# Optimization experiments

Hardware: AMD Instinct MI355X
Metric: run time of the kernel (lower is better)

Reference implementation:

```python
import jax, jax.numpy as jnp
import numpy as np

B, N, D = 4, 1024, 1024
H = 16
RS, RC = 32, 32
MLP = int(D * 4.0)
EPS = 1e-6


def _ln(x):
    # LayerNorm with no scale/bias (flax defaults: eps=1e-6)
    m = jnp.mean(x, axis=-1, keepdims=True)
    v = jnp.mean(jnp.square(x - m), axis=-1, keepdims=True)
    return (x - m) * jax.lax.rsqrt(v + EPS)


def _rms(x, scale):
    rms = jnp.sqrt(jnp.mean(jnp.square(x), axis=-1, keepdims=True) + EPS)
    return scale * x / rms


def _modulate(x, shift, scale):
    return x * (1 + scale[:, None]) + shift[:, None]


def setup_inputs() -> dict:
    key = jax.random.key(0)
    ks = jax.random.split(key, 20)
    s = 0.02
    return {
        'x': jax.random.normal(ks[0], (B, N, D), jnp.float32),
        'c': jax.random.normal(ks[1], (B, D), jnp.float32),
        'cls_token': jax.random.normal(ks[2], (B, D), jnp.float32),
        'Wc': jax.random.normal(ks[3], (D, 6 * D), jnp.float32) * s,
        'bc': jax.random.normal(ks[4], (6 * D,), jnp.float32) * s,
        'Wqkv': jax.random.normal(ks[5], (D, 3 * D), jnp.float32) * s,
        'bqkv': jnp.zeros((3 * D,), jnp.float32),
        'Wo': jax.random.normal(ks[6], (D, D), jnp.float32) * s,
        'bo': jnp.zeros((D,), jnp.float32),
        'A_s': jax.random.normal(ks[7], (D, RS), jnp.float32) * s,
        'B_s': jax.random.normal(ks[8], (RS, D), jnp.float32) * s,
        'rms_s_scale': jnp.ones((D,), jnp.float32),
        'C_r': jax.random.normal(ks[9], (D, RC), jnp.float32) * s,
        'D_r': jax.random.normal(ks[10], (RC, D), jnp.float32) * s,
        'rms_c_scale': jnp.ones((D,), jnp.float32),
        'W1': jax.random.normal(ks[11], (D, MLP), jnp.float32) * s,
        'b1': jnp.zeros((MLP,), jnp.float32),
        'W2': jax.random.normal(ks[12], (MLP, D), jnp.float32) * s,
        'b2': jnp.zeros((D,), jnp.float32),
    }


def reference(x, c, cls_token, Wc, bc, Wqkv, bqkv, Wo, bo, A_s, B_s,
              rms_s_scale, C_r, D_r, rms_c_scale, W1, b1, W2, b2):
    hd = D // H
    # AdaLN conditioning
    c_proj = jax.nn.silu(c) @ Wc + bc                    # (B, 6D)
    shift_a, scale_a, gate_a, shift_m, scale_m, gate_m = jnp.split(c_proj, 6, axis=-1)

    # Self-attention branch
    x_norm = _modulate(_ln(x), shift_a, scale_a)         # (B, N, D)
    qkv = x_norm @ Wqkv + bqkv                           # (B, N, 3D)
    q, k, v = jnp.split(qkv, 3, axis=-1)
    q = q.reshape(B, N, H, hd).transpose(0, 2, 1, 3)     # (B, H, N, hd)
    k = k.reshape(B, N, H, hd).transpose(0, 2, 1, 3)
    v = v.reshape(B, N, H, hd).transpose(0, 2, 1, 3)
    attn_w = jax.nn.softmax(jnp.einsum('bhqd,bhkd->bhqk', q, k) * hd ** (-0.5), axis=-1)
    attn_out = jnp.einsum('bhqk,bhkd->bhqd', attn_w, v)
    attn_out = attn_out.transpose(0, 2, 1, 3).reshape(B, N, D)
    attn_out = attn_out @ Wo + bo
    Y = x + gate_a[:, None] * attn_out

    # Self-gram low-rank branch (residual)
    gram_s = (x @ A_s) @ B_s                             # (B, N, D)
    X_prime = _rms(gram_s, rms_s_scale) + Y

    # Cross-gram branch via CLS token (no residual)
    u_c = cls_token[:, :, None] * C_r[None]              # (B, D, RC)
    v_c = jnp.einsum('bnd,bdr->bnr', X_prime, u_c)       # (B, N, RC)
    gram_c = v_c @ D_r                                   # (B, N, D)
    Z = _rms(gram_c, rms_c_scale)

    # MLP branch
    z_norm = _modulate(_ln(Z), shift_m, scale_m)
    h = jax.nn.gelu(z_norm @ W1 + b1) @ W2 + b2
    return Z + gate_m[:, None] * h
```

## Files before the change

### kernel.cpp

```cpp
#include <hip/hip_runtime.h>
#include <stdint.h>

typedef float  f32x4  __attribute__((ext_vector_type(4)));
typedef int    i32x4  __attribute__((ext_vector_type(4)));
typedef __bf16 bf16x4 __attribute__((ext_vector_type(4)));

#define D_    1024
#define SIXD  6144
#define QSCALE 0.18033688011112042f

#define BAR() asm volatile("s_barrier" ::: "memory")

__device__ __forceinline__ void mfma16(const i32x4 &a, const i32x4 &b, f32x4 &c) {
  asm("v_mfma_f32_16x16x32_bf16 %0, %1, %2, %0" : "+v"(c) : "v"(a), "v"(b));
}

__device__ __forceinline__ void gload_lds16(const void* g, void* l) {
  __builtin_amdgcn_global_load_lds(
      (const __attribute__((address_space(1))) uint32_t*)g,
      (__attribute__((address_space(3))) uint32_t*)l, 16, 0, 0);
}

__global__ __launch_bounds__(256)
void cond_gemm(const float* __restrict__ c, const float* __restrict__ Wc,
               const float* __restrict__ bc, float* __restrict__ cproj)
{
  __shared__ float sc[4096];
  __shared__ float tp[8][4][32];
  int tid = threadIdx.x;
  for (int i = tid; i < 4096; i += 256) {
    float v = c[i];
    sc[i] = v / (1.f + __expf(-v));
  }
  __syncthreads();
  int colo = tid & 31, kseg = tid >> 5;
  int col = blockIdx.x * 32 + colo;
  float a0 = 0.f, a1 = 0.f, a2 = 0.f, a3 = 0.f;
  for (int k = kseg * 128; k < kseg * 128 + 128; k++) {
    float w = Wc[(size_t)k * SIXD + col];
    a0 += sc[k] * w; a1 += sc[1024 + k] * w;
    a2 += sc[2048 + k] * w; a3 += sc[3072 + k] * w;
  }
  tp[kseg][0][colo] = a0; tp[kseg][1][colo] = a1;
  tp[kseg][2][colo] = a2; tp[kseg][3][colo] = a3;
  __syncthreads();
  if (kseg == 0) {
#pragma unroll
    for (int b = 0; b < 4; b++) {
      float s = bc[col];
#pragma unroll
      for (int g = 0; g < 8; g++) s += tp[g][b][colo];
      cproj[b * SIXD + col] = s;
    }
  }
}

__global__ __launch_bounds__(256)
void transpose_all(const float* __restrict__ Wqkv, const float* __restrict__ Wo,
                   const float* __restrict__ W1, const float* __restrict__ W2,
                   __bf16* __restrict__ Wqkvt, __bf16* __restrict__ Wot,
                   __bf16* __restrict__ W1t, __bf16* __restrict__ W2t)
{
  __shared__ __bf16 t[64][65];
  int bid = blockIdx.x;
  const float* W; __bf16* Wt; int Kdim, Ndim, lb;
  if (bid < 768)       { W = Wqkv; Wt = Wqkvt; Kdim = 1024; Ndim = 3072; lb = bid; }
  else if (bid < 1024) { W = Wo;   Wt = Wot;   Kdim = 1024; Ndim = 1024; lb = bid - 768; }
  else if (bid < 2048) { W = W1;   Wt = W1t;   Kdim = 1024; Ndim = 4096; lb = bid - 1024; }
  else                 { W = W2;   Wt = W2t;   Kdim = 4096; Ndim = 1024; lb = bid - 2048; }
  int ntn = Ndim >> 6;
  int kt = lb / ntn, nt = lb % ntn;
  int tid = threadIdx.x;
  const float* src = W + (size_t)(kt * 64) * Ndim + nt * 64;
#pragma unroll
  for (int i = 0; i < 4; i++) {
    int k = i * 16 + (tid >> 4);
    int c4 = tid & 15;
    float4 v = ((const float4*)(src + (size_t)k * Ndim))[c4];
    t[k][c4 * 4 + 0] = (__bf16)v.x; t[k][c4 * 4 + 1] = (__bf16)v.y;
    t[k][c4 * 4 + 2] = (__bf16)v.z; t[k][c4 * 4 + 3] = (__bf16)v.w;
  }
  __syncthreads();
  __bf16* dst = Wt + (size_t)(nt * 64) * Kdim + kt * 64;
  int n = tid >> 2, ks = (tid & 3) * 16;
  bf16x4 o0, o1, o2, o3;
#pragma unroll
  for (int j = 0; j < 4; j++) {
    o0[j] = t[ks + j][n];      o1[j] = t[ks + 4 + j][n];
    o2[j] = t[ks + 8 + j][n];  o3[j] = t[ks + 12 + j][n];
  }
  __bf16* dp = dst + (size_t)n * Kdim + ks;
  *(bf16x4*)(dp) = o0; *(bf16x4*)(dp + 4) = o1;
  *(bf16x4*)(dp + 8) = o2; *(bf16x4*)(dp + 12) = o3;
}

__global__ __launch_bounds__(256)
void transpose_v(const __bf16* __restrict__ qkv, __bf16* __restrict__ Vt)
{
  __shared__ __bf16 t[32][33];
  int bid = blockIdx.x;
  int dt = bid & 1, nt = (bid >> 1) & 31, bh = bid >> 6;
  int b = bh >> 4, h = bh & 15;
  int x = threadIdx.x & 31, yq = threadIdx.x >> 5;
  const __bf16* src = qkv + ((size_t)(b * 1024 + nt * 32)) * 3072 + 2048 + h * 64 + dt * 32;
#pragma unroll
  for (int i = 0; i < 4; i++) {
    int row = yq * 4 + i;
    t[row][x] = src[(size_t)row * 3072 + x];
  }
  __syncthreads();
  __bf16* dst = Vt + ((size_t)(bh * 64 + dt * 32)) * 1024 + nt * 32;
#pragma unroll
  for (int i = 0; i < 4; i++) {
    int drow = yq * 4 + i;
    dst[(size_t)drow * 1024 + x] = t[x][drow];
  }
}

__global__ __launch_bounds__(256)
void ln_mod(const float* __restrict__ X, const float* __restrict__ cproj,
            int shift_off, int scale_off, __bf16* __restrict__ Out)
{
  int row = blockIdx.x;
  int b = row >> 10;
  int tid = threadIdx.x;
  const float4* xr = (const float4*)(X + (size_t)row * D_);
  float4 v = xr[tid];
  float s  = v.x + v.y + v.z + v.w;
  float s2 = v.x * v.x + v.y * v.y + v.z * v.z + v.w * v.w;
#pragma unroll
  for (int off = 1; off < 64; off <<= 1) {
    s  += __shfl_xor(s,  off, 64);
    s2 += __shfl_xor(s2, off, 64);
  }
  __shared__ float red[8];
  int wave = tid >> 6, lane = tid & 63;
  if (lane == 0) { red[wave] = s; red[4 + wave] = s2; }
  __syncthreads();
  s  = red[0] + red[1] + red[2] + red[3];
  s2 = red[4] + red[5] + red[6] + red[7];
  float mean = s * (1.f / D_);
  float var  = s2 * (1.f / D_) - mean * mean;
  float rstd = rsqrtf(var + 1e-6f);
  const float4* sh = (const float4*)(cproj + b * SIXD + shift_off);
  const float4* sc = (const float4*)(cproj + b * SIXD + scale_off);
  float4 shv = sh[tid], scv = sc[tid];
  bf16x4 o;
  o[0] = (__bf16)((v.x - mean) * rstd * (1.f + scv.x) + shv.x);
  o[1] = (__bf16)((v.y - mean) * rstd * (1.f + scv.y) + shv.y);
  o[2] = (__bf16)((v.z - mean) * rstd * (1.f + scv.z) + shv.z);
  o[3] = (__bf16)((v.w - mean) * rstd * (1.f + scv.w) + shv.w);
  *(bf16x4*)(Out + (size_t)row * D_ + tid * 4) = o;
}

template<int EPI, int NBUF>
__global__ __launch_bounds__(256)
void gemm_bt(const __bf16* __restrict__ A, const __bf16* __restrict__ Bt,
             const float* __restrict__ bias, const float* __restrict__ cproj,
             int gate_off, const float* __restrict__ resid,
             void* __restrict__ Cout, void* __restrict__ Cout2,
             void* __restrict__ Cout3, void* __restrict__ Cout4,
             int M, int N, int K, int SK)
{
  __shared__ __align__(16) __bf16 As[NBUF * 128 * 32];
  __shared__ __align__(16) __bf16 Bs[NBUF * 128 * 32];
  const int PD = NBUF - 1;
  int tilesN = N >> 7, tilesM = M >> 7;
  int npersk = tilesM * tilesN;
  int sk = blockIdx.x / npersk;
  int rest = blockIdx.x % npersk;
  int cpx = npersk >> 3;
  rest = (rest & 7) * cpx + (rest >> 3);
  int bm = rest / tilesN, bn = rest % tilesN;
  int Klen = K / SK, Kstart = sk * Klen;

  int tid = threadIdx.x;
  int lane = tid & 63, wave = tid >> 6;
  int lr = lane & 15, lg = lane >> 4;
  int wm = (wave >> 1) << 6, wn = (wave & 1) << 6;

  f32x4 acc[4][4] = {};

  int sr = tid >> 2, skb = tid & 3;
  int scol = ((skb ^ ((sr >> 1) & 3)) * 8);
  const __bf16* pa = A + (size_t)((bm << 7) + sr) * K + Kstart + scol;
  const __bf16* pb = Bt + (size_t)((bn << 7) + sr) * K + Kstart + scol;
  const size_t rstep = (size_t)64 * K;
  __bf16* la = As + tid * 8;
  __bf16* lb = Bs + tid * 8;

  auto STAGE = [&](int buf, int k0) {
    int bo = buf * 4096;
    gload_lds16(pa + k0, la + bo);
    gload_lds16(pa + rstep + k0, la + bo + 2048);
    gload_lds16(pb + k0, lb + bo);
    gload_lds16(pb + rstep + k0, lb + bo + 2048);
  };

  int nt = Klen >> 5;
#pragma unroll
  for (int p = 0; p < PD; p++) STAGE(p, p * 32);

  for (int t = 0; t < nt; t++) {
    if (t + PD < nt) STAGE((t + PD) % NBUF, (t + PD) * 32);
    int ahead = nt - 1 - t; if (ahead > PD) ahead = PD;
    if (ahead >= 3)      asm volatile("s_waitcnt vmcnt(12)" ::: "memory");
    else if (ahead == 2) asm volatile("s_waitcnt vmcnt(8)" ::: "memory");
    else if (ahead == 1) asm volatile("s_waitcnt vmcnt(4)" ::: "memory");
    else                 asm volatile("s_waitcnt vmcnt(0)" ::: "memory");
    BAR();
    const __bf16* Ac = As + (t % NBUF) * 4096;
    const __bf16* Bc = Bs + (t % NBUF) * 4096;
    i32x4 af[4], bfv[4];
#pragma unroll
    for (int m = 0; m < 4; m++) {
      int row = wm + m * 16 + lr;
      af[m] = *(const i32x4*)(Ac + row * 32 + ((lg ^ ((row >> 1) & 3)) * 8));
    }
#pragma unroll
    for (int n = 0; n < 4; n++) {
      int row = wn + n * 16 + lr;
      bfv[n] = *(const i32x4*)(Bc + row * 32 + ((lg ^ ((row >> 1) & 3)) * 8));
    }
    asm volatile("s_waitcnt lgkmcnt(0)" ::: "memory");
    __builtin_amdgcn_sched_barrier(0);
    BAR();
    __builtin_amdgcn_s_setprio(1);
#pragma unroll
    for (int m = 0; m < 4; m++)
#pragma unroll
      for (int n = 0; n < 4; n++)
        mfma16(af[m], bfv[n], acc[m][n]);
    __builtin_amdgcn_s_setprio(0);
  }
  asm volatile("s_waitcnt vmcnt(0)" ::: "memory");
  asm volatile("s_nop 7\n\ts_nop 7" ::);

  __bf16* Pp = nullptr;
  if (EPI == 3) {
    if (sk == 0)      Pp = (__bf16*)Cout;
    else if (sk == 1) Pp = (__bf16*)Cout2;
    else if (sk == 2) Pp = (__bf16*)Cout3;
    else              Pp = (__bf16*)Cout4;
  }

  int row0 = (bm << 7) + wm;
  int col0 = (bn << 7) + wn;
#pragma unroll
  for (int m = 0; m < 4; m++) {
#pragma unroll
    for (int n = 0; n < 4; n++) {
      int cc = col0 + n * 16 + lr;
      float bv = (EPI == 3) ? 0.f : bias[cc];
#pragma unroll
      for (int r = 0; r < 4; r++) {
        int row = row0 + m * 16 + (lg << 2) + r;
        float v = acc[m][n][r] + bv;
        size_t idx = (size_t)row * N + cc;
        if (EPI == 0) {
          ((__bf16*)Cout)[idx] = (__bf16)v;
        } else if (EPI == 1) {
          int b = row >> 10;
          float g = cproj[b * SIXD + gate_off + cc];
          ((float*)Cout)[idx] = resid[idx] + g * v;
        } else if (EPI == 2) {
          float u = 0.7978845608028654f * (v + 0.044715f * v * v * v);
          u = fminf(fmaxf(u, -15.f), 15.f);
          float e = __expf(2.f * u);
          float th = (e - 1.f) / (e + 1.f);
          ((__bf16*)Cout)[idx] = (__bf16)(0.5f * v * (1.f + th));
        } else if (EPI == 4) {
          float scq = (cc < 1024) ? QSCALE : 1.f;
          ((__bf16*)Cout)[idx] = (__bf16)(v * scq);
        } else {
          Pp[idx] = (__bf16)v;
        }
      }
    }
  }
}

__global__ __launch_bounds__(256)
void reduce_w2(const __bf16* __restrict__ P0, const __bf16* __restrict__ P1,
               const __bf16* __restrict__ P2, const __bf16* __restrict__ P3,
               const float* __restrict__ bias, const float* __restrict__ cproj,
               float* __restrict__ Out)
{
  int row = blockIdx.x;
  int b = row >> 10;
  int tid = threadIdx.x;
  size_t base = (size_t)row * D_ + tid * 4;
  bf16x4 a0 = *(const bf16x4*)(P0 + base);
  bf16x4 a1 = *(const bf16x4*)(P1 + base);
  bf16x4 a2 = *(const bf16x4*)(P2 + base);
  bf16x4 a3 = *(const bf16x4*)(P3 + base);
  f32x4 s;
#pragma unroll
  for (int i = 0; i < 4; i++)
    s[i] = ((float)a0[i] + (float)a1[i]) + ((float)a2[i] + (float)a3[i]);
  f32x4 bz = *(const f32x4*)(bias + tid * 4);
  f32x4 g  = *(const f32x4*)(cproj + b * SIXD + 5120 + tid * 4);
  f32x4 z  = *(const f32x4*)(Out + base);
  *(f32x4*)(Out + base) = z + g * (s + bz);
}

__global__ __launch_bounds__(512, 4)
void attn_flash(const __bf16* __restrict__ qkv, const __bf16* __restrict__ Vt,
                __bf16* __restrict__ O)
{
  __shared__ __align__(16) __bf16 Kl[2][64 * 64];
  __shared__ __align__(16) __bf16 Vl[2][64 * 64];
  __shared__ __align__(16) __bf16 Pl[8][16 * 64];

  int bid = ((blockIdx.x & 7) << 6) | (blockIdx.x >> 3);
  int qt = bid & 7, h = (bid >> 3) & 15, b = bid >> 7;
  int tid = threadIdx.x, wave = tid >> 6, lane = tid & 63;
  int lr = lane & 15, lg = lane >> 4;

  size_t tok0 = (size_t)b * 1024;
  int qrow = qt * 128 + wave * 16 + lr;
  const __bf16* qptr = qkv + (tok0 + qrow) * 3072 + h * 64;
  i32x4 qf0 = *(const i32x4*)(qptr + lg * 8);
  i32x4 qf1 = *(const i32x4*)(qptr + 32 + lg * 8);

  float l_acc[4] = {0.f, 0.f, 0.f, 0.f};
  f32x4 oacc[4] = {};

  const __bf16* kbase = qkv + tok0 * 3072 + 1024 + h * 64;
  const __bf16* vbase = Vt + ((size_t)(b * 16 + h) * 64) * 1024;

  int skey = tid >> 3, sdb = tid & 7;
  const __bf16* ksrc = kbase + (size_t)skey * 3072 + ((sdb ^ (skey & 7)) * 8);
  const __bf16* vsrc = vbase + (size_t)skey * 1024 + ((sdb ^ (skey & 7)) * 8);
  __bf16* klp = &Kl[0][0] + tid * 8;
  __bf16* vlp = &Vl[0][0] + tid * 8;
  __bf16* pl = &Pl[wave][0];

  auto STAGE = [&](int buf, int kk) {
    gload_lds16(ksrc + (size_t)kk * 3072, klp + buf * 4096);
    gload_lds16(vsrc + kk, vlp + buf * 4096);
  };

  STAGE(0, 0);
  int cur = 0;
  for (int k0 = 0; k0 < 1024; k0 += 64) {
    int kn = (k0 + 64 < 1024) ? (k0 + 64) : k0;
    STAGE(cur ^ 1, kn);
    asm volatile("s_waitcnt vmcnt(2)" ::: "memory");
    BAR();
    const __bf16* K_ = &Kl[cur][0];
    const __bf16* V_ = &Vl[cur][0];

    f32x4 s[4];
    __builtin_amdgcn_s_setprio(1);
#pragma unroll
    for (int n = 0; n < 4; n++) {
      int key = n * 16 + lr;
      int kx = key & 7;
      i32x4 kf0 = *(const i32x4*)(K_ + key * 64 + ((lg ^ kx) * 8));
      i32x4 kf1 = *(const i32x4*)(K_ + key * 64 + (((4 + lg) ^ kx) * 8));
      f32x4 sa = {0.f, 0.f, 0.f, 0.f};
      mfma16(qf0, kf0, sa);
      mfma16(qf1, kf1, sa);
      s[n] = sa;
    }
    __builtin_amdgcn_s_setprio(0);

#pragma unroll
    for (int n = 0; n < 4; n++)
#pragma unroll
      for (int r = 0; r < 4; r++)
        s[n][r] = exp2f(s[n][r]);
#pragma unroll
    for (int r = 0; r < 4; r++)
      l_acc[r] += (s[0][r] + s[1][r]) + (s[2][r] + s[3][r]);

#pragma unroll
    for (int n = 0; n < 4; n++)
#pragma unroll
      for (int r = 0; r < 4; r++) {
        int prow = lg * 4 + r;
        int key = n * 16 + lr;
        int idx = prow * 64 + (((key >> 3) ^ (prow & 7)) * 8) + (key & 7);
        pl[idx] = (__bf16)s[n][r];
      }
    asm volatile("s_waitcnt lgkmcnt(0)" ::: "memory");
    __builtin_amdgcn_sched_barrier(0);
    i32x4 pf0 = *(const i32x4*)(pl + lr * 64 + ((lg ^ (lr & 7)) * 8));
    i32x4 pf1 = *(const i32x4*)(pl + lr * 64 + (((4 + lg) ^ (lr & 7)) * 8));

    __builtin_amdgcn_s_setprio(1);
#pragma unroll
    for (int dt = 0; dt < 4; dt++) {
      int vrow = dt * 16 + lr, rx = vrow & 7;
      i32x4 vf0 = *(const i32x4*)(V_ + vrow * 64 + ((lg ^ rx) * 8));
      i32x4 vf1 = *(const i32x4*)(V_ + vrow * 64 + (((4 + lg) ^ rx) * 8));
      mfma16(pf0, vf0, oacc[dt]);
      mfma16(pf1, vf1, oacc[dt]);
    }
    __builtin_amdgcn_s_setprio(0);
    asm volatile("s_waitcnt lgkmcnt(0)" ::: "memory");
    __builtin_amdgcn_sched_barrier(0);
    BAR();
    cur ^= 1;
  }
  asm volatile("s_waitcnt vmcnt(0)" ::: "memory");
  asm volatile("s_nop 7\n\ts_nop 7" ::);

  float rinv[4];
#pragma unroll
  for (int r = 0; r < 4; r++) {
    float v = l_acc[r];
#pragma unroll
    for (int off = 1; off < 16; off <<= 1) v += __shfl_xor(v, off, 64);
    rinv[r] = 1.f / v;
  }

  int orow = qt * 128 + wave * 16 + (lg << 2);
#pragma unroll
  for (int dt = 0; dt < 4; dt++)
#pragma unroll
    for (int r = 0; r < 4; r++) {
      float v = oacc[dt][r] * rinv[r];
      O[(tok0 + orow + r) * 1024 + h * 64 + dt * 16 + lr] = (__bf16)v;
    }
}

__global__ __launch_bounds__(256)
void gram_fused(const float* __restrict__ X, const float* __restrict__ Y,
                const float* __restrict__ cls,
                const float* __restrict__ A_s, const float* __restrict__ B_s,
                const float* __restrict__ rms_s,
                const float* __restrict__ C_r, const float* __restrict__ D_r,
                const float* __restrict__ rms_c,
                const float* __restrict__ cproj,
                float* __restrict__ Z, __bf16* __restrict__ Znorm)
{
  __shared__ float xs[4][D_];
  __shared__ float tp[8][4][32];
  __shared__ float t1[4][32];
  __shared__ float red[4][4];
  __shared__ float red2[4][4][2];
  int row0 = blockIdx.x * 4;
  int b = row0 >> 10;
  int tid = threadIdx.x;
  int wv = tid >> 6;

  f32x4 cv = *(const f32x4*)(cls + (size_t)b * D_ + tid * 4);
  f32x4 yv[4];
#pragma unroll
  for (int rr = 0; rr < 4; rr++) {
    ((f32x4*)xs[rr])[tid] = *(const f32x4*)(X + (size_t)(row0 + rr) * D_ + tid * 4);
    yv[rr] = *(const f32x4*)(Y + (size_t)(row0 + rr) * D_ + tid * 4);
  }
  __syncthreads();

  {
    int r = tid & 31, seg = tid >> 5;
    float a0 = 0.f, a1 = 0.f, a2 = 0.f, a3 = 0.f;
    const float* ap = A_s + r;
    for (int d = seg * 128; d < seg * 128 + 128; d++) {
      float w = ap[d * 32];
      a0 += xs[0][d] * w; a1 += xs[1][d] * w;
      a2 += xs[2][d] * w; a3 += xs[3][d] * w;
    }
    tp[seg][0][r] = a0; tp[seg][1][r] = a1; tp[seg][2][r] = a2; tp[seg][3][r] = a3;
  }
  __syncthreads();
  if (tid < 128) {
    int rr = tid >> 5, r = tid & 31;
    float sv = 0.f;
#pragma unroll
    for (int g = 0; g < 8; g++) sv += tp[g][rr][r];
    t1[rr][r] = sv;
  }
  __syncthreads();

  f32x4 g[4] = {};
  for (int r = 0; r < 32; r++) {
    f32x4 bv = *(const f32x4*)(B_s + (size_t)r * D_ + tid * 4);
    g[0] += t1[0][r] * bv; g[1] += t1[1][r] * bv;
    g[2] += t1[2][r] * bv; g[3] += t1[3][r] * bv;
  }
  float ssl[4];
#pragma unroll
  for (int rr = 0; rr < 4; rr++)
    ssl[rr] = g[rr][0]*g[rr][0] + g[rr][1]*g[rr][1] + g[rr][2]*g[rr][2] + g[rr][3]*g[rr][3];
#pragma unroll
  for (int off = 1; off < 64; off <<= 1)
#pragma unroll
    for (int rr = 0; rr < 4; rr++) ssl[rr] += __shfl_xor(ssl[rr], off, 64);
  if ((tid & 63) == 0) {
#pragma unroll
    for (int rr = 0; rr < 4; rr++) red[wv][rr] = ssl[rr];
  }
  __syncthreads();
  {
    f32x4 scv = *(const f32x4*)(rms_s + tid * 4);
#pragma unroll
    for (int rr = 0; rr < 4; rr++) {
      float ss = red[0][rr] + red[1][rr] + red[2][rr] + red[3][rr];
      float rs = rsqrtf(ss * (1.f / D_) + 1e-6f);
      f32x4 xp = scv * g[rr] * rs + yv[rr];
      ((f32x4*)xs[rr])[tid] = xp * cv;
    }
  }
  __syncthreads();

  {
    int r = tid & 31, seg = tid >> 5;
    float a0 = 0.f, a1 = 0.f, a2 = 0.f, a3 = 0.f;
    const float* cp = C_r + r;
    for (int d = seg * 128; d < seg * 128 + 128; d++) {
      float w = cp[d * 32];
      a0 += xs[0][d] * w; a1 += xs[1][d] * w;
      a2 += xs[2][d] * w; a3 += xs[3][d] * w;
    }
    tp[seg][0][r] = a0; tp[seg][1][r] = a1; tp[seg][2][r] = a2; tp[seg][3][r] = a3;
  }
  __syncthreads();
  if (tid < 128) {
    int rr = tid >> 5, r = tid & 31;
    float sv = 0.f;
#pragma unroll
    for (int g2i = 0; g2i < 8; g2i++) sv += tp[g2i][rr][r];
    t1[rr][r] = sv;
  }
  __syncthreads();

  f32x4 g2[4] = {};
  for (int r = 0; r < 32; r++) {
    f32x4 bv = *(const f32x4*)(D_r + (size_t)r * D_ + tid * 4);
    g2[0] += t1[0][r] * bv; g2[1] += t1[1][r] * bv;
    g2[2] += t1[2][r] * bv; g2[3] += t1[3][r] * bv;
  }
#pragma unroll
  for (int rr = 0; rr < 4; rr++)
    ssl[rr] = g2[rr][0]*g2[rr][0] + g2[rr][1]*g2[rr][1] + g2[rr][2]*g2[rr][2] + g2[rr][3]*g2[rr][3];
#pragma unroll
  for (int off = 1; off < 64; off <<= 1)
#pragma unroll
    for (int rr = 0; rr < 4; rr++) ssl[rr] += __shfl_xor(ssl[rr], off, 64);
  if ((tid & 63) == 0) {
#pragma unroll
    for (int rr = 0; rr < 4; rr++) red[wv][rr] = ssl[rr];
  }
  __syncthreads();
  f32x4 z[4];
  {
    f32x4 scv = *(const f32x4*)(rms_c + tid * 4);
#pragma unroll
    for (int rr = 0; rr < 4; rr++) {
      float ss = red[0][rr] + red[1][rr] + red[2][rr] + red[3][rr];
      float rs = rsqrtf(ss * (1.f / D_) + 1e-6f);
      z[rr] = scv * g2[rr] * rs;
    }
  }

  float s1l[4], s2l[4];
#pragma unroll
  for (int rr = 0; rr < 4; rr++) {
    s1l[rr] = z[rr][0] + z[rr][1] + z[rr][2] + z[rr][3];
    s2l[rr] = z[rr][0]*z[rr][0] + z[rr][1]*z[rr][1] + z[rr][2]*z[rr][2] + z[rr][3]*z[rr][3];
  }
#pragma unroll
  for (int off = 1; off < 64; off <<= 1)
#pragma unroll
    for (int rr = 0; rr < 4; rr++) {
      s1l[rr] += __shfl_xor(s1l[rr], off, 64);
      s2l[rr] += __shfl_xor(s2l[rr], off, 64);
    }
  if ((tid & 63) == 0) {
#pragma unroll
    for (int rr = 0; rr < 4; rr++) { red2[wv][rr][0] = s1l[rr]; red2[wv][rr][1] = s2l[rr]; }
  }
  __syncthreads();
  f32x4 shv = *(const f32x4*)(cproj + b * SIXD + 3072 + tid * 4);
  f32x4 scm = *(const f32x4*)(cproj + b * SIXD + 4096 + tid * 4);
#pragma unroll
  for (int rr = 0; rr < 4; rr++) {
    float S  = red2[0][rr][0] + red2[1][rr][0] + red2[2][rr][0] + red2[3][rr][0];
    float S2 = red2[0][rr][1] + red2[1][rr][1] + red2[2][rr][1] + red2[3][rr][1];
    float mean = S * (1.f / D_);
    float var  = S2 * (1.f / D_) - mean * mean;
    float rstd = rsqrtf(var + 1e-6f);
    f32x4 zn = (z[rr] - mean) * rstd * (scm + 1.f) + shv;
    *(f32x4*)(Z + (size_t)(row0 + rr) * D_ + tid * 4) = z[rr];
    bf16x4 o;
#pragma unroll
    for (int i = 0; i < 4; i++) o[i] = (__bf16)zn[i];
    *(bf16x4*)(Znorm + (size_t)(row0 + rr) * D_ + tid * 4) = o;
  }
}

extern "C" void kernel_launch(void* const* d_in, const int* in_sizes, int n_in,
                              void* d_out, int out_size, void* d_ws, size_t ws_size,
                              hipStream_t stream)
{
  const float* x     = (const float*)d_in[0];
  const float* c     = (const float*)d_in[1];
  const float* cls   = (const float*)d_in[2];
  const float* Wc    = (const float*)d_in[3];
  const float* bc    = (const float*)d_in[4];
  const float* Wqkv  = (const float*)d_in[5];
  const float* bqkv  = (const float*)d_in[6];
  const float* Wo    = (const float*)d_in[7];
  const float* bo    = (const float*)d_in[8];
  const float* A_s   = (const float*)d_in[9];
  const float* B_s   = (const float*)d_in[10];
  const float* rms_s = (const float*)d_in[11];
  const float* C_r   = (const float*)d_in[12];
  const float* D_r   = (const float*)d_in[13];
  const float* rms_c = (const float*)d_in[14];
  const float* W1    = (const float*)d_in[15];
  const float* b1    = (const float*)d_in[16];
  const float* W2    = (const float*)d_in[17];
  const float* b2    = (const float*)d_in[18];
  float* out = (float*)d_out;

  float* ws = (float*)d_ws;
  __bf16* Wqkvt = (__bf16*)(ws + 0);
  __bf16* Wot   = (__bf16*)(ws + 1572864);
  __bf16* W1t   = (__bf16*)(ws + 2097152);
  __bf16* W2t   = (__bf16*)(ws + 4194304);
  float*  cproj = ws + 6291456;
  __bf16* xnorm = (__bf16*)(ws + 6316032);
  __bf16* qkv   = (__bf16*)(ws + 8413184);
  __bf16* Vt    = (__bf16*)(ws + 14704640);
  __bf16* h1    = (__bf16*)(ws + 8413184);
  __bf16* attno = (__bf16*)(ws + 16801792);
  float*  Ybuf  = ws + 18898944;
  __bf16* P0 = (__bf16*)(ws + 0);
  __bf16* P1 = (__bf16*)(ws + 2097152);
  __bf16* P2 = (__bf16*)(ws + 16801792);
  __bf16* P3 = (__bf16*)(ws + 18898944);

  cond_gemm<<<192, 256, 0, stream>>>(c, Wc, bc, cproj);
  transpose_all<<<3072, 256, 0, stream>>>(Wqkv, Wo, W1, W2, Wqkvt, Wot, W1t, W2t);
  ln_mod<<<4096, 256, 0, stream>>>(x, cproj, 0, 1024, xnorm);
  gemm_bt<4, 3><<<768, 256, 0, stream>>>(xnorm, Wqkvt, bqkv, nullptr, 0, nullptr,
                                         qkv, nullptr, nullptr, nullptr,
                                         4096, 3072, 1024, 1);
  transpose_v<<<4096, 256, 0, stream>>>(qkv, Vt);
  attn_flash<<<512, 512, 0, stream>>>(qkv, Vt, attno);
  gemm_bt<1, 4><<<256, 256, 0, stream>>>(attno, Wot, bo, cproj, 2048, x,
                                         Ybuf, nullptr, nullptr, nullptr,
                                         4096, 1024, 1024, 1);
  gram_fused<<<1024, 256, 0, stream>>>(x, Ybuf, cls, A_s, B_s, rms_s,
                                       C_r, D_r, rms_c, cproj, out, xnorm);
  gemm_bt<2, 2><<<1024, 256, 0, stream>>>(xnorm, W1t, b1, nullptr, 0, nullptr,
                                          h1, nullptr, nullptr, nullptr,
                                          4096, 4096, 1024, 1);
  gemm_bt<3, 2><<<1024, 256, 0, stream>>>(h1, W2t, nullptr, nullptr, 0, nullptr,
                                          P0, P1, P2, P3, 4096, 1024, 4096, 4);
  reduce_w2<<<4096, 256, 0, stream>>>(P0, P1, P2, P3, b2, cproj, out);
}
```

Before: 284.4 us.

## Add 256x256-tile 8-wave GEMM with interleaved LDS prefetch for QKV and MLP

Adds a new GEMM kernel that uses 256x256 output tiles and 512 threads, with double-buffered LDS filled by direct global-to-LDS loads. Loads for the next K-tile are issued in quarter slices between MFMA phases, and an XOR-swizzled LDS layout avoids bank conflicts. The QKV, W1 and W2 GEMMs now use this kernel, which raises data reuse per block. In exchange there are far fewer blocks (192-256 on a 256-CU part), so some CUs may sit idle, and register pressure is high.

```diff
diff --git a/kernel.cpp b/kernel.cpp
--- a/kernel.cpp
+++ b/kernel.cpp
@@ -280,6 +280,188 @@
   }
 }
 
+template<int EPI>
+__global__ __launch_bounds__(512, 2)
+void gemm256(const __bf16* __restrict__ A, const __bf16* __restrict__ Bt,
+             const float* __restrict__ bias,
+             void* __restrict__ Cout, void* __restrict__ Cout2,
+             void* __restrict__ Cout3, void* __restrict__ Cout4,
+             int M, int N, int K, int SK)
+{
+  __shared__ __align__(16) __bf16 As[2 * 16384];
+  __shared__ __align__(16) __bf16 Bs[2 * 16384];
+  int tilesN = N >> 8, tilesM = M >> 8;
+  int npersk = tilesM * tilesN;
+  int sk = blockIdx.x / npersk;
+  int rest = blockIdx.x % npersk;
+  int cpx = npersk >> 3;
+  rest = (rest & 7) * cpx + (rest >> 3);
+  int bm = rest / tilesN, bn = rest % tilesN;
+  int Klen = K / SK, Kstart = sk * Klen;
+  int nt = Klen >> 6;
+
+  int tid = threadIdx.x;
+  int lane = tid & 63, wave = tid >> 6;
+  int lr = lane & 15, lg = lane >> 4;
+  int wr = wave >> 2, wc = wave & 3;
+
+  f32x4 acc[8][4] = {};
+
+  int srow = tid >> 3;
+  int schunk = (tid & 7) ^ (srow & 7);
+  const __bf16* pa = A  + (size_t)((bm << 8) + srow) * K + Kstart + schunk * 8;
+  const __bf16* pb = Bt + (size_t)((bn << 8) + srow) * K + Kstart + schunk * 8;
+  __bf16* la = As + tid * 8;
+  __bf16* lb = Bs + tid * 8;
+
+  auto SA = [&](int t, int h, int j) {
+    gload_lds16(pa + (size_t)(h * 128 + j * 64) * K + t * 64,
+                la + (t & 1) * 16384 + h * 8192 + j * 4096);
+  };
+  auto SB = [&](int t, int h, int j) {
+    gload_lds16(pb + (size_t)(h * 128 + j * 64) * K + t * 64,
+                lb + (t & 1) * 16384 + h * 8192 + j * 4096);
+  };
+
+  SA(0,0,0); SA(0,0,1); SA(0,1,0); SA(0,1,1);
+  SB(0,0,0); SB(0,0,1); SB(0,1,0); SB(0,1,1);
+  SB(1,0,0); SB(1,0,1); SB(1,1,0); SB(1,1,1);
+  asm volatile("s_waitcnt vmcnt(4)" ::: "memory");
+  BAR();
+
+  int cc0 = ((lg ^ (lr & 7)) << 4);
+  int cc1 = cc0 ^ 64;
+  const char* aA = (const char*)As + (wr * 128 + lr) * 128;
+  const char* aB = (const char*)Bs + (wc * 64 + lr) * 128;
+
+  i32x4 af[4][2], b0[2][2], b1[2][2];
+  for (int t = 0; t < nt; t++) {
+    const char* Ab = aA + (t & 1) * 32768;
+    const char* Bb = aB + (t & 1) * 32768;
+
+#pragma unroll
+    for (int m = 0; m < 4; m++) {
+      af[m][0] = *(const i32x4*)(Ab + m * 2048 + cc0);
+      af[m][1] = *(const i32x4*)(Ab + m * 2048 + cc1);
+    }
+#pragma unroll
+    for (int n = 0; n < 2; n++) {
+      b0[n][0] = *(const i32x4*)(Bb + n * 2048 + cc0);
+      b0[n][1] = *(const i32x4*)(Bb + n * 2048 + cc1);
+    }
+    if (t + 1 < nt) { SA(t + 1, 0, 0); SA(t + 1, 0, 1); }
+    BAR();
+    asm volatile("s_waitcnt lgkmcnt(0)" ::: "memory");
+    __builtin_amdgcn_sched_barrier(0);
+    __builtin_amdgcn_s_setprio(1);
+#pragma unroll
+    for (int m = 0; m < 4; m++)
+#pragma unroll
+      for (int n = 0; n < 2; n++) {
+        mfma16(af[m][0], b0[n][0], acc[m][n]);
+        mfma16(af[m][1], b0[n][1], acc[m][n]);
+      }
+    __builtin_amdgcn_s_setprio(0);
+    BAR();
+
+#pragma unroll
+    for (int n = 0; n < 2; n++) {
+      b1[n][0] = *(const i32x4*)(Bb + 4096 + n * 2048 + cc0);
+      b1[n][1] = *(const i32x4*)(Bb + 4096 + n * 2048 + cc1);
+    }
+    if (t + 1 < nt) { SA(t + 1, 1, 0); SA(t + 1, 1, 1); }
+    BAR();
+    asm volatile("s_waitcnt lgkmcnt(0)" ::: "memory");
+    __builtin_amdgcn_sched_barrier(0);
+    __builtin_amdgcn_s_setprio(1);
+#pragma unroll
+    for (int m = 0; m < 4; m++)
+#pragma unroll
+      for (int n = 0; n < 2; n++) {
+        mfma16(af[m][0], b1[n][0], acc[m][2 + n]);
+        mfma16(af[m][1], b1[n][1], acc[m][2 + n]);
+      }
+    __builtin_amdgcn_s_setprio(0);
+    BAR();
+
+#pragma unroll
+    for (int m = 0; m < 4; m++) {
+      af[m][0] = *(const i32x4*)(Ab + 8192 + m * 2048 + cc0);
+      af[m][1] = *(const i32x4*)(Ab + 8192 + m * 2048 + cc1);
+    }
+    if (t + 2 < nt) { SB(t + 2, 0, 0); SB(t + 2, 0, 1); }
+    BAR();
+    asm volatile("s_waitcnt lgkmcnt(0)" ::: "memory");
+    __builtin_amdgcn_sched_barrier(0);
+    __builtin_amdgcn_s_setprio(1);
+#pragma unroll
+    for (int m = 0; m < 4; m++)
+#pragma unroll
+      for (int n = 0; n < 2; n++) {
+        mfma16(af[m][0], b1[n][0], acc[4 + m][2 + n]);
+        mfma16(af[m][1], b1[n][1], acc[4 + m][2 + n]);
+      }
+    __builtin_amdgcn_s_setprio(0);
+    BAR();
+
+    if (t + 2 < nt) {
+      SB(t + 2, 1, 0); SB(t + 2, 1, 1);
+      asm volatile("s_waitcnt vmcnt(4)" ::: "memory");
+    } else {
+      asm volatile("s_waitcnt vmcnt(0)" ::: "memory");
+    }
+    BAR();
+    __builtin_amdgcn_s_setprio(1);
+#pragma unroll
+    for (int m = 0; m < 4; m++)
+#pragma unroll
+      for (int n = 0; n < 2; n++) {
+        mfma16(af[m][0], b0[n][0], acc[4 + m][n]);
+        mfma16(af[m][1], b0[n][1], acc[4 + m][n]);
+      }
+    __builtin_amdgcn_s_setprio(0);
+    BAR();
+  }
+  asm volatile("s_nop 7\n\ts_nop 7" ::);
+
+  __bf16* Pp = nullptr;
+  if (EPI == 3) {
+    if (sk == 0)      Pp = (__bf16*)Cout;
+    else if (sk == 1) Pp = (__bf16*)Cout2;
+    else if (sk == 2) Pp = (__bf16*)Cout3;
+    else              Pp = (__bf16*)Cout4;
+  }
+
+  int row0 = (bm << 8) + wr * 128;
+  int col0 = (bn << 8) + wc * 64;
+#pragma unroll
+  for (int m = 0; m < 8; m++) {
+#pragma unroll
+    for (int n = 0; n < 4; n++) {
+      int cc = col0 + n * 16 + lr;
+      float bv = (EPI == 3) ? 0.f : bias[cc];
+#pragma unroll
+      for (int r = 0; r < 4; r++) {
+        int row = row0 + m * 16 + (lg << 2) + r;
+        float v = acc[m][n][r] + bv;
+        size_t idx = (size_t)row * N + cc;
+        if (EPI == 2) {
+          float u = 0.7978845608028654f * (v + 0.044715f * v * v * v);
+          u = fminf(fmaxf(u, -15.f), 15.f);
+          float e = __expf(2.f * u);
+          float th = (e - 1.f) / (e + 1.f);
+          ((__bf16*)Cout)[idx] = (__bf16)(0.5f * v * (1.f + th));
+        } else if (EPI == 4) {
+          float scq = (cc < 1024) ? QSCALE : 1.f;
+          ((__bf16*)Cout)[idx] = (__bf16)(v * scq);
+        } else {
+          Pp[idx] = (__bf16)v;
+        }
+      }
+    }
+  }
+}
+
 __global__ __launch_bounds__(256)
 void reduce_w2(const __bf16* __restrict__ P0, const __bf16* __restrict__ P1,
                const __bf16* __restrict__ P2, const __bf16* __restrict__ P3,
@@ -638,9 +820,9 @@
   cond_gemm<<<192, 256, 0, stream>>>(c, Wc, bc, cproj);
   transpose_all<<<3072, 256, 0, stream>>>(Wqkv, Wo, W1, W2, Wqkvt, Wot, W1t, W2t);
   ln_mod<<<4096, 256, 0, stream>>>(x, cproj, 0, 1024, xnorm);
-  gemm_bt<4, 3><<<768, 256, 0, stream>>>(xnorm, Wqkvt, bqkv, nullptr, 0, nullptr,
-                                         qkv, nullptr, nullptr, nullptr,
-                                         4096, 3072, 1024, 1);
+  gemm256<4><<<192, 512, 0, stream>>>(xnorm, Wqkvt, bqkv,
+                                      qkv, nullptr, nullptr, nullptr,
+                                      4096, 3072, 1024, 1);
   transpose_v<<<4096, 256, 0, stream>>>(qkv, Vt);
   attn_flash<<<512, 512, 0, stream>>>(qkv, Vt, attno);
   gemm_bt<1, 4><<<256, 256, 0, stream>>>(attno, Wot, bo, cproj, 2048, x,
@@ -648,10 +830,10 @@
                                          4096, 1024, 1024, 1);
   gram_fused<<<1024, 256, 0, stream>>>(x, Ybuf, cls, A_s, B_s, rms_s,
                                        C_r, D_r, rms_c, cproj, out, xnorm);
-  gemm_bt<2, 2><<<1024, 256, 0, stream>>>(xnorm, W1t, b1, nullptr, 0, nullptr,
-                                          h1, nullptr, nullptr, nullptr,
-                                          4096, 4096, 1024, 1);
-  gemm_bt<3, 2><<<1024, 256, 0, stream>>>(h1, W2t, nullptr, nullptr, 0, nullptr,
-                                          P0, P1, P2, P3, 4096, 1024, 4096, 4);
+  gemm256<2><<<256, 512, 0, stream>>>(xnorm, W1t, b1,
+                                      h1, nullptr, nullptr, nullptr,
+                                      4096, 4096, 1024, 1);
+  gemm256<3><<<256, 512, 0, stream>>>(h1, W2t, nullptr,
+                                      P0, P1, P2, P3, 4096, 1024, 4096, 4);
   reduce_w2<<<4096, 256, 0, stream>>>(P0, P1, P2, P3, b2, cproj, out);
 }
```

Result: faster. 272.8 us (-4.1%).

## Add 256x256-tile triple-buffered GEMM for QKV/MLP and merge prep kernels

Applied to the files above, without the earlier changes.

Introduces a new 512-thread GEMM kernel with 256x256 output tiles, triple-buffered direct-to-LDS loads, swizzled LDS layout, accumulators held in AGPRs, and an XCD-aware tile remap. It replaces the QKV, W1 and W2 GEMMs, with W2 split-K over four partials. The cond GEMM and weight transposes are merged into one launch. The larger tiles cut global and LDS traffic per FLOP, but they produce only 192-256 blocks, which risks underfilling the GPU's compute units. The large accumulator set also adds register pressure.

```diff
diff --git a/kernel.cpp b/kernel.cpp
--- a/kernel.cpp
+++ b/kernel.cpp
@@ -13,6 +13,9 @@
 
 __device__ __forceinline__ void mfma16(const i32x4 &a, const i32x4 &b, f32x4 &c) {
   asm("v_mfma_f32_16x16x32_bf16 %0, %1, %2, %0" : "+v"(c) : "v"(a), "v"(b));
+}
+__device__ __forceinline__ void mfma16a(const i32x4 &a, const i32x4 &b, f32x4 &c) {
+  asm("v_mfma_f32_16x16x32_bf16 %0, %1, %2, %0" : "+a"(c) : "v"(a), "v"(b));
 }
 
 __device__ __forceinline__ void gload_lds16(const void* g, void* l) {
@@ -22,47 +25,46 @@
 }
 
 __global__ __launch_bounds__(256)
-void cond_gemm(const float* __restrict__ c, const float* __restrict__ Wc,
-               const float* __restrict__ bc, float* __restrict__ cproj)
+void prep(const float* __restrict__ c, const float* __restrict__ Wc,
+          const float* __restrict__ bc, float* __restrict__ cproj,
+          const float* __restrict__ Wqkv, const float* __restrict__ Wo,
+          const float* __restrict__ W1, const float* __restrict__ W2,
+          __bf16* __restrict__ Wqkvt, __bf16* __restrict__ Wot,
+          __bf16* __restrict__ W1t, __bf16* __restrict__ W2t)
 {
   __shared__ float sc[4096];
   __shared__ float tp[8][4][32];
+  __shared__ __bf16 tt[64][65];
   int tid = threadIdx.x;
-  for (int i = tid; i < 4096; i += 256) {
-    float v = c[i];
-    sc[i] = v / (1.f + __expf(-v));
-  }
-  __syncthreads();
-  int colo = tid & 31, kseg = tid >> 5;
-  int col = blockIdx.x * 32 + colo;
-  float a0 = 0.f, a1 = 0.f, a2 = 0.f, a3 = 0.f;
-  for (int k = kseg * 128; k < kseg * 128 + 128; k++) {
-    float w = Wc[(size_t)k * SIXD + col];
-    a0 += sc[k] * w; a1 += sc[1024 + k] * w;
-    a2 += sc[2048 + k] * w; a3 += sc[3072 + k] * w;
-  }
-  tp[kseg][0][colo] = a0; tp[kseg][1][colo] = a1;
-  tp[kseg][2][colo] = a2; tp[kseg][3][colo] = a3;
-  __syncthreads();
-  if (kseg == 0) {
-#pragma unroll
-    for (int b = 0; b < 4; b++) {
-      float s = bc[col];
-#pragma unroll
-      for (int g = 0; g < 8; g++) s += tp[g][b][colo];
-      cproj[b * SIXD + col] = s;
-    }
-  }
-}
-
-__global__ __launch_bounds__(256)
-void transpose_all(const float* __restrict__ Wqkv, const float* __restrict__ Wo,
-                   const float* __restrict__ W1, const float* __restrict__ W2,
-                   __bf16* __restrict__ Wqkvt, __bf16* __restrict__ Wot,
-                   __bf16* __restrict__ W1t, __bf16* __restrict__ W2t)
-{
-  __shared__ __bf16 t[64][65];
-  int bid = blockIdx.x;
+  if (blockIdx.x < 192) {
+    for (int i = tid; i < 4096; i += 256) {
+      float v = c[i];
+      sc[i] = v / (1.f + __expf(-v));
+    }
+    __syncthreads();
+    int colo = tid & 31, kseg = tid >> 5;
+    int col = blockIdx.x * 32 + colo;
+    float a0 = 0.f, a1 = 0.f, a2 = 0.f, a3 = 0.f;
+    for (int k = kseg * 128; k < kseg * 128 + 128; k++) {
+      float w = Wc[(size_t)k * SIXD + col];
+      a0 += sc[k] * w; a1 += sc[1024 + k] * w;
+      a2 += sc[2048 + k] * w; a3 += sc[3072 + k] * w;
+    }
+    tp[kseg][0][colo] = a0; tp[kseg][1][colo] = a1;
+    tp[kseg][2][colo] = a2; tp[kseg][3][colo] = a3;
+    __syncthreads();
+    if (kseg == 0) {
+#pragma unroll
+      for (int b = 0; b < 4; b++) {
+        float s = bc[col];
+#pragma unroll
+        for (int g = 0; g < 8; g++) s += tp[g][b][colo];
+        cproj[b * SIXD + col] = s;
+      }
+    }
+    return;
+  }
+  int bid = blockIdx.x - 192;
   const float* W; __bf16* Wt; int Kdim, Ndim, lb;
   if (bid < 768)       { W = Wqkv; Wt = Wqkvt; Kdim = 1024; Ndim = 3072; lb = bid; }
   else if (bid < 1024) { W = Wo;   Wt = Wot;   Kdim = 1024; Ndim = 1024; lb = bid - 768; }
@@ -70,15 +72,14 @@
   else                 { W = W2;   Wt = W2t;   Kdim = 4096; Ndim = 1024; lb = bid - 2048; }
   int ntn = Ndim >> 6;
   int kt = lb / ntn, nt = lb % ntn;
-  int tid = threadIdx.x;
   const float* src = W + (size_t)(kt * 64) * Ndim + nt * 64;
 #pragma unroll
   for (int i = 0; i < 4; i++) {
     int k = i * 16 + (tid >> 4);
     int c4 = tid & 15;
     float4 v = ((const float4*)(src + (size_t)k * Ndim))[c4];
-    t[k][c4 * 4 + 0] = (__bf16)v.x; t[k][c4 * 4 + 1] = (__bf16)v.y;
-    t[k][c4 * 4 + 2] = (__bf16)v.z; t[k][c4 * 4 + 3] = (__bf16)v.w;
+    tt[k][c4 * 4 + 0] = (__bf16)v.x; tt[k][c4 * 4 + 1] = (__bf16)v.y;
+    tt[k][c4 * 4 + 2] = (__bf16)v.z; tt[k][c4 * 4 + 3] = (__bf16)v.w;
   }
   __syncthreads();
   __bf16* dst = Wt + (size_t)(nt * 64) * Kdim + kt * 64;
@@ -86,8 +87,8 @@
   bf16x4 o0, o1, o2, o3;
 #pragma unroll
   for (int j = 0; j < 4; j++) {
-    o0[j] = t[ks + j][n];      o1[j] = t[ks + 4 + j][n];
-    o2[j] = t[ks + 8 + j][n];  o3[j] = t[ks + 12 + j][n];
+    o0[j] = tt[ks + j][n];      o1[j] = tt[ks + 4 + j][n];
+    o2[j] = tt[ks + 8 + j][n];  o3[j] = tt[ks + 12 + j][n];
   }
   __bf16* dp = dst + (size_t)n * Kdim + ks;
   *(bf16x4*)(dp) = o0; *(bf16x4*)(dp + 4) = o1;
@@ -280,6 +281,137 @@
   }
 }
 
+template<int EPI, int NT, int KD>
+__global__ __launch_bounds__(512, 2)
+void gemm256(const __bf16* __restrict__ A, const __bf16* __restrict__ Bt,
+             const float* __restrict__ bias,
+             void* __restrict__ Cout, void* __restrict__ Cout2,
+             void* __restrict__ Cout3, void* __restrict__ Cout4,
+             int M, int N)
+{
+  __shared__ __align__(16) __bf16 As[3 * 8192];
+  __shared__ __align__(16) __bf16 Bs[3 * 8192];
+  int tilesN = N >> 8, tilesM = M >> 8;
+  int npersk = tilesM * tilesN;
+  int sk = blockIdx.x / npersk;
+  int rest = blockIdx.x % npersk;
+  int cpx = npersk >> 3;
+  rest = (rest & 7) * cpx + (rest >> 3);
+  int bm = rest / tilesN, bn = rest % tilesN;
+  int Kstart = sk * (NT * 32);
+
+  int tid = threadIdx.x;
+  int lane = tid & 63, wave = tid >> 6;
+  int lr = lane & 15, lg = lane >> 4;
+  int wr = wave >> 2, wc = wave & 3;
+
+  f32x4 acc[8][4] = {};
+
+  int srow = tid >> 2;
+  int schunk = (tid & 3) ^ ((srow >> 1) & 3);
+  const __bf16* pa = A  + (size_t)((bm << 8) + srow) * KD + Kstart + schunk * 8;
+  const __bf16* pb = Bt + (size_t)((bn << 8) + srow) * KD + Kstart + schunk * 8;
+  __bf16* la = As + tid * 8;
+  __bf16* lb = Bs + tid * 8;
+
+  auto SA = [&](int t, int h, int slot) {
+    gload_lds16(pa + (size_t)(h * 128) * KD + t * 32, la + slot + h * 4096);
+  };
+  auto SB = [&](int t, int h, int slot) {
+    gload_lds16(pb + (size_t)(h * 128) * KD + t * 32, lb + slot + h * 4096);
+  };
+
+  SA(0, 0, 0); SA(0, 1, 0); SB(0, 0, 0); SB(0, 1, 0);
+  SA(1, 0, 8192); SA(1, 1, 8192); SB(1, 0, 8192); SB(1, 1, 8192);
+  asm volatile("s_waitcnt vmcnt(4)" ::: "memory");
+  BAR();
+
+  int cc = ((lg ^ ((lr >> 1) & 3)) << 4);
+  const char* aA = (const char*)As + (wr * 128 + lr) * 64 + cc;
+  const char* aB = (const char*)Bs + (wc * 64 + lr) * 64 + cc;
+
+  int o0 = 0, o1 = 16384, o2 = 32768;
+
+  for (int t = 0; t < NT; t++) {
+    const char* Ab = aA + o0;
+    const char* Bb = aB + o0;
+
+    if (t + 2 < NT) {
+      SA(t + 2, 0, o2 >> 1); SA(t + 2, 1, o2 >> 1);
+      SB(t + 2, 0, o2 >> 1); SB(t + 2, 1, o2 >> 1);
+    }
+
+    i32x4 av[4], bv[4];
+#pragma unroll
+    for (int n = 0; n < 4; n++) bv[n] = *(const i32x4*)(Bb + n * 1024);
+#pragma unroll
+    for (int m = 0; m < 4; m++) av[m] = *(const i32x4*)(Ab + m * 1024);
+    __builtin_amdgcn_s_setprio(1);
+#pragma unroll
+    for (int m = 0; m < 4; m++)
+#pragma unroll
+      for (int n = 0; n < 4; n++)
+        mfma16a(av[m], bv[n], acc[m][n]);
+    __builtin_amdgcn_s_setprio(0);
+
+    i32x4 av2[4];
+#pragma unroll
+    for (int m = 0; m < 4; m++) av2[m] = *(const i32x4*)(Ab + 4096 + m * 1024);
+    __builtin_amdgcn_s_setprio(1);
+#pragma unroll
+    for (int m = 0; m < 4; m++)
+#pragma unroll
+      for (int n = 0; n < 4; n++)
+        mfma16a(av2[m], bv[n], acc[4 + m][n]);
+    __builtin_amdgcn_s_setprio(0);
+
+    if (t + 2 < NT)      asm volatile("s_waitcnt vmcnt(4)" ::: "memory");
+    else if (t + 1 < NT) asm volatile("s_waitcnt vmcnt(0)" ::: "memory");
+    if (t + 1 < NT) BAR();
+
+    int tmp = o0; o0 = o1; o1 = o2; o2 = tmp;
+  }
+  asm volatile("s_waitcnt lgkmcnt(0)" ::: "memory");
+  asm volatile("s_nop 7\n\ts_nop 7" ::);
+
+  __bf16* Pp = nullptr;
+  if (EPI == 3) {
+    if (sk == 0)      Pp = (__bf16*)Cout;
+    else if (sk == 1) Pp = (__bf16*)Cout2;
+    else if (sk == 2) Pp = (__bf16*)Cout3;
+    else              Pp = (__bf16*)Cout4;
+  }
+
+  int row0 = (bm << 8) + wr * 128;
+  int col0 = (bn << 8) + wc * 64;
+#pragma unroll
+  for (int m = 0; m < 8; m++) {
+#pragma unroll
+    for (int n = 0; n < 4; n++) {
+      int cc2 = col0 + n * 16 + lr;
+      float bvv = (EPI == 3) ? 0.f : bias[cc2];
+#pragma unroll
+      for (int r = 0; r < 4; r++) {
+        int row = row0 + m * 16 + (lg << 2) + r;
+        float v = acc[m][n][r] + bvv;
+        size_t idx = (size_t)row * N + cc2;
+        if (EPI == 2) {
+          float u = 0.7978845608028654f * (v + 0.044715f * v * v * v);
+          u = fminf(fmaxf(u, -15.f), 15.f);
+          float e = __expf(2.f * u);
+          float th = (e - 1.f) / (e + 1.f);
+          ((__bf16*)Cout)[idx] = (__bf16)(0.5f * v * (1.f + th));
+        } else if (EPI == 4) {
+          float scq = (cc2 < 1024) ? QSCALE : 1.f;
+          ((__bf16*)Cout)[idx] = (__bf16)(v * scq);
+        } else {
+          Pp[idx] = (__bf16)v;
+        }
+      }
+    }
+  }
+}
+
 __global__ __launch_bounds__(256)
 void reduce_w2(const __bf16* __restrict__ P0, const __bf16* __restrict__ P1,
                const __bf16* __restrict__ P2, const __bf16* __restrict__ P3,
@@ -635,12 +767,12 @@
   __bf16* P2 = (__bf16*)(ws + 16801792);
   __bf16* P3 = (__bf16*)(ws + 18898944);
 
-  cond_gemm<<<192, 256, 0, stream>>>(c, Wc, bc, cproj);
-  transpose_all<<<3072, 256, 0, stream>>>(Wqkv, Wo, W1, W2, Wqkvt, Wot, W1t, W2t);
+  prep<<<3264, 256, 0, stream>>>(c, Wc, bc, cproj,
+                                 Wqkv, Wo, W1, W2, Wqkvt, Wot, W1t, W2t);
   ln_mod<<<4096, 256, 0, stream>>>(x, cproj, 0, 1024, xnorm);
-  gemm_bt<4, 3><<<768, 256, 0, stream>>>(xnorm, Wqkvt, bqkv, nullptr, 0, nullptr,
-                                         qkv, nullptr, nullptr, nullptr,
-                                         4096, 3072, 1024, 1);
+  gemm256<4, 32, 1024><<<192, 512, 0, stream>>>(xnorm, Wqkvt, bqkv,
+                                                qkv, nullptr, nullptr, nullptr,
+                                                4096, 3072);
   transpose_v<<<4096, 256, 0, stream>>>(qkv, Vt);
   attn_flash<<<512, 512, 0, stream>>>(qkv, Vt, attno);
   gemm_bt<1, 4><<<256, 256, 0, stream>>>(attno, Wot, bo, cproj, 2048, x,
@@ -648,10 +780,10 @@
                                          4096, 1024, 1024, 1);
   gram_fused<<<1024, 256, 0, stream>>>(x, Ybuf, cls, A_s, B_s, rms_s,
                                        C_r, D_r, rms_c, cproj, out, xnorm);
-  gemm_bt<2, 2><<<1024, 256, 0, stream>>>(xnorm, W1t, b1, nullptr, 0, nullptr,
-                                          h1, nullptr, nullptr, nullptr,
-                                          4096, 4096, 1024, 1);
-  gemm_bt<3, 2><<<1024, 256, 0, stream>>>(h1, W2t, nullptr, nullptr, 0, nullptr,
-                                          P0, P1, P2, P3, 4096, 1024, 4096, 4);
+  gemm256<2, 32, 1024><<<256, 512, 0, stream>>>(xnorm, W1t, b1,
+                                                h1, nullptr, nullptr, nullptr,
+                                                4096, 4096);
+  gemm256<3, 32, 4096><<<256, 512, 0, stream>>>(h1, W2t, nullptr,
+                                                P0, P1, P2, P3, 4096, 1024);
   reduce_w2<<<4096, 256, 0, stream>>>(P0, P1, P2, P3, b2, cproj, out);
 }
```

New measurement: 288.9 us. About the same (+1.6%).
